# Kernel optimization log

Hardware: AMD Instinct MI355X
Metric: run time of the kernel (lower is better)

Reference implementation:

```python
import jax, jax.numpy as jnp
import numpy as np

D = 640          # feature dim (x_dim)
C = 64           # number of classes
N = 1024         # support samples (16 shots/class)
Q = 2048         # query samples
REG = 0.3        # reg_param


def setup_inputs() -> dict:
    key = jax.random.key(0)
    k0, k1, k2, k3, k4 = jax.random.split(key, 5)
    X = jax.random.normal(k0, (N, D), jnp.float32)
    y = (jnp.arange(N) % C).astype(jnp.int32)          # every class populated
    Xq = jax.random.normal(k1, (Q, D), jnp.float32)
    # learnable prior parameters (perturbed from the torch init so grads are nontrivial)
    m = 0.02 * jax.random.normal(k2, (1, D), jnp.float32)
    kappa = jnp.array([0.1], jnp.float32)
    nu = jnp.array([float(D)], jnp.float32)
    triu_diag = 1.0 + 0.05 * jax.random.normal(k3, (D,), jnp.float32)
    triu_lower = jnp.eye(D, dtype=jnp.float32) + 0.05 * jax.random.normal(k4, (D, D), jnp.float32)
    return {"X": X, "y": y, "Xq": Xq, "m": m, "kappa": kappa, "nu": nu,
            "triu_diag": triu_diag, "triu_lower": triu_lower}


def reference(X, y, Xq, m, kappa, nu, triu_diag, triu_lower):
    # strictly-lower-triangular mask: triu(ones, 1).T
    mask = jnp.triu(jnp.ones((D, D), X.dtype), 1).T
    L = jnp.diag(jnp.abs(triu_diag)) + triu_lower * mask          # Cholesky-like factor
    kappa_ = jnp.abs(kappa[0]) + 1e-6
    nu_ = jnp.maximum(nu[0], D - 1 + 1e-6)

    onehot = jax.nn.one_hot(y, C, dtype=X.dtype)                   # [N, C]
    Nc = onehot.sum(0)                                             # [C]
    mean_c = (onehot.T @ X) / Nc[:, None]                          # [C, D]
    # MAP posterior mean per class
    w = Nc / (kappa_ + Nc)
    mu = (1.0 - w)[:, None] * m + w[:, None] * mean_c              # [C, D]

    # per-class second moment: S_c = sum_{y=c} x x^T (segmented X^T X)
    Xc = onehot.T[:, :, None] * X[None, :, :]                      # [C, N, D]
    S = jnp.einsum('cnd,ne->cde', Xc, X)                           # [C, D, D]

    LLt = L @ L.T
    mm = m.T @ m                                                   # [D, D]
    mu_outer = jnp.einsum('cd,ce->cde', mu, mu)
    sigma = (LLt[None] + S + kappa_ * mm[None]
             - (kappa_ + Nc)[:, None, None] * mu_outer)
    sigma = sigma / (nu_ + Nc + D + 2)[:, None, None]
    sigma_inv = jnp.linalg.inv(sigma)
    sigma_inv = (1.0 - REG) * sigma_inv + REG * jnp.eye(D, dtype=X.dtype)

    # batched Mahalanobis quadratic form: -(x - mu_c)^T Sinv_c (x - mu_c)
    diff = Xq[:, None, :] - mu[None, :, :]                         # [Q, C, D]
    dist = jnp.einsum('qcd,cde,qce->qc', diff, sigma_inv, diff)
    return -dist
```

## Files before the change

kernel.cpp:

```cpp
#include <hip/hip_runtime.h>
#include <hip/hip_bf16.h>


#define D 640
#define C 64
#define NSUP 1024
#define Q 2048
#define KMAX 16
#define R18 18
#define VROWS (C * R18)
#define YROWS 3137
#define YPAD 3200
#define NEXT 704

typedef __attribute__((ext_vector_type(8))) short bf16x8;
typedef __attribute__((ext_vector_type(4))) float floatx4;

__device__ __forceinline__ unsigned short f2bf(float x) {
    unsigned int u = __float_as_uint(x);
    unsigned int r = u + 0x7FFFu + ((u >> 16) & 1u);
    return (unsigned short)(r >> 16);
}

__device__ __forceinline__ void pack4(const float* vv, unsigned short* hp, unsigned short* lp) {
#pragma unroll
    for (int i = 0; i < 4; ++i) {
        unsigned short hb = f2bf(vv[i]);
        float hf = __uint_as_float((unsigned int)hb << 16);
        hp[i] = hb;
        lp[i] = f2bf(vv[i] - hf);
    }
}

__device__ __forceinline__ void rownorm_body(const float* __restrict__ A, int ld,
                                             float* __restrict__ out, int gw, int lane) {
    const float* row = A + (size_t)gw * ld;
    float s = 0.f;
    for (int d = lane; d < D; d += 64) { float v = row[d]; s += v * v; }
#pragma unroll
    for (int off = 32; off; off >>= 1) s += __shfl_xor(s, off);
    if (lane == 0) out[gw] = s;
}

#define BZCH (640 * 640 / 8)
#define AZCH (63 * 640 / 8)
__global__ void k_setup(const int* __restrict__ y, const float* __restrict__ kappa,
                        const float* __restrict__ nu, const float* __restrict__ diag,
                        int* __restrict__ cnt, int* __restrict__ idx,
                        float* __restrict__ sc, float* __restrict__ rd,
                        int* __restrict__ rowmap,
                        unsigned short* __restrict__ Ah, unsigned short* __restrict__ Al,
                        unsigned short* __restrict__ Bh, unsigned short* __restrict__ Bl) {
    int tid = threadIdx.x;
    if (blockIdx.x > 0) {
        int id = (blockIdx.x - 1) * 256 + tid;
        const uint4 z = {0u, 0u, 0u, 0u};
        if (id < BZCH) ((uint4*)Bh)[id] = z;
        else if (id < 2 * BZCH) ((uint4*)Bl)[id - BZCH] = z;
        else if (id < 2 * BZCH + AZCH) ((uint4*)(Ah + (size_t)YROWS * D))[id - 2 * BZCH] = z;
        else if (id < 2 * BZCH + 2 * AZCH) ((uint4*)(Al + (size_t)YROWS * D))[id - 2 * BZCH - AZCH] = z;
        return;
    }
    __shared__ int lc[C];
    if (tid < C) lc[tid] = 0;
    __syncthreads();
    for (int n = tid; n < NSUP; n += 256) {
        int c = y[n];
        int k = atomicAdd(&lc[c], 1);
        if (k < KMAX) idx[c * KMAX + k] = n;
    }
    __syncthreads();
    for (int d = tid; d < D; d += 256) rd[d] = 1.0f / fabsf(diag[d]);
    if (tid < C) {
        int n = lc[tid]; if (n > KMAX) n = KMAX;
        cnt[tid] = n;
        float kap = fabsf(kappa[0]) + 1e-6f;
        float nuv = fmaxf(nu[0], (float)(D - 1) + 1e-6f);
        float Ncf = (float)n;
        sc[64 + tid]  = Ncf / (kap + Ncf);
        sc[128 + tid] = nuv + Ncf + (float)(D + 2);
        sc[192 + tid] = -1.0f / (kap + Ncf);
        if (tid == 0) { sc[0] = kap; sc[1] = nuv; }
    }
    __syncthreads();
    for (int i = tid; i < VROWS; i += 256) {
        int c = i / R18, j = i - c * R18;
        int nc = lc[c] < KMAX ? lc[c] : KMAX;
        int rm;
        if (j == 0) rm = Q + NSUP;
        else if (j <= KMAX) rm = (j - 1 < nc) ? Q + idx[c * KMAX + j - 1] : -1;
        else rm = Q + NSUP + 1 + c;
        rowmap[i] = rm;
    }
}

__global__ __launch_bounds__(256) void k_dinv_mu(
        const float* __restrict__ tlow, const float* __restrict__ rd,
        float* __restrict__ Linv,
        const float* __restrict__ X, const float* __restrict__ m,
        const int* __restrict__ cnt, const int* __restrict__ idx,
        const float* __restrict__ sc, float* __restrict__ mu,
        const float* __restrict__ Xq,
        unsigned short* __restrict__ Ah, unsigned short* __restrict__ Al,
        unsigned short* __restrict__ Bh, unsigned short* __restrict__ Bl,
        float* __restrict__ a0) {
    __shared__ float Lst[128 * 128];
    int tid = threadIdx.x;
    int bid = blockIdx.x;
    if (bid < 160) {
        int b = bid >> 5;
        int j = ((bid & 31) << 2) + (tid >> 6);
        int lane = tid & 63;
        int bB = b * 128;
        {
            float4 tv[16];
            float rv[16];
#pragma unroll
            for (int u = 0; u < 16; ++u) {
                int e = tid + u * 256;
                int c4 = (e & 31) * 4, r = e >> 5;
                tv[u] = *(const float4*)(tlow + (size_t)(bB + r) * D + bB + c4);
                rv[u] = rd[bB + r];
            }
#pragma unroll
            for (int u = 0; u < 16; ++u) {
                int e = tid + u * 256;
                int c4 = (e & 31) * 4, r = e >> 5;
                float vv[4] = {tv[u].x, tv[u].y, tv[u].z, tv[u].w};
#pragma unroll
                for (int t = 0; t < 4; ++t) {
                    int c = c4 + t;
                    float v;
                    if (r == c) v = 1.0f;
                    else if (r > c) v = rv[u] * vv[t];
                    else v = 0.f;
                    Lst[c * 128 + (r ^ (c & 63))] = v;
                }
            }
        }
        __syncthreads();
        float rd0 = rd[bB + lane], rd1 = rd[bB + 64 + lane];
        float acc0 = 0.f, acc1 = 0.f, zz0 = 0.f, zz1 = 0.f;
        for (int i = j; i < 128; ++i) {
            int ri = i >> 6, il = i & 63;
            float av = (ri == 0) ? acc0 : acc1;
            float ai = __shfl(av, il);
            float zi = (i == j) ? __shfl((ri == 0) ? rd0 : rd1, il) : -ai;
            int sw = i & 63;
            float l0 = Lst[i * 128 + (lane ^ sw)];
            float l1 = Lst[i * 128 + 64 + (lane ^ sw)];
            if (lane > i) acc0 += l0 * zi;
            if (64 + lane > i) acc1 += l1 * zi;
            if (lane == i) zz0 = zi;
            if (64 + lane == i) zz1 = zi;
        }
        Linv[(size_t)(bB + lane) * D + bB + j] = zz0;
        Linv[(size_t)(bB + 64 + lane) * D + bB + j] = zz1;
        unsigned short h0 = f2bf(zz0);
        float hf0 = __uint_as_float((unsigned int)h0 << 16);
        Bh[(size_t)(bB + lane) * D + bB + j] = h0;
        Bl[(size_t)(bB + lane) * D + bB + j] = f2bf(zz0 - hf0);
        unsigned short h1 = f2bf(zz1);
        float hf1 = __uint_as_float((unsigned int)h1 << 16);
        Bh[(size_t)(bB + 64 + lane) * D + bB + j] = h1;
        Bl[(size_t)(bB + 64 + lane) * D + bB + j] = f2bf(zz1 - hf1);
    } else if (bid < 320) {
        int u = (bid - 160) * 2 + (tid >> 7);
        int c = u / 5, by = u - c * 5;
        int d = by * 128 + (tid & 127);
        int n = cnt[c];
        float s = 0.f;
        for (int k = 0; k < n; ++k) s += X[(size_t)idx[c * KMAX + k] * D + d];
        float w = sc[64 + c];
        float mean = (n > 0) ? s / (float)n : 0.f;
        float val = (1.f - w) * m[d] + w * mean;
        mu[(size_t)c * D + d] = val;
        unsigned short hb = f2bf(val);
        float hf = __uint_as_float((unsigned int)hb << 16);
        unsigned short lb = f2bf(val - hf);
        Ah[(size_t)(Q + NSUP + 1 + c) * D + d] = hb;
        Al[(size_t)(Q + NSUP + 1 + c) * D + d] = lb;
        Bh[(size_t)(D + c) * D + d] = hb;
        Bl[(size_t)(D + c) * D + d] = lb;
    } else if (bid < 2240) {
        int gid = (bid - 320) * 256 + tid;
        int row = gid / 160, c = (gid - row * 160) * 4;
        float4 v = (row < Q) ? *(const float4*)(Xq + (size_t)row * D + c)
                             : *(const float4*)(X + (size_t)(row - Q) * D + c);
        float vv[4] = {v.x, v.y, v.z, v.w};
        ushort4 h, l;
        pack4(vv, (unsigned short*)&h, (unsigned short*)&l);
        *(ushort4*)(Ah + (size_t)row * D + c) = h;
        *(ushort4*)(Al + (size_t)row * D + c) = l;
    } else if (bid == 2240) {
        if (tid < 160) {
            int c = tid * 4;
            float4 v = *(const float4*)(m + c);
            float vv[4] = {v.x, v.y, v.z, v.w};
            ushort4 h, l;
            pack4(vv, (unsigned short*)&h, (unsigned short*)&l);
            *(ushort4*)(Ah + (size_t)(Q + NSUP) * D + c) = h;
            *(ushort4*)(Al + (size_t)(Q + NSUP) * D + c) = l;
        }
    } else {
        int gw = ((bid - 2241) * 256 + tid) >> 6;
        rownorm_body(Xq, D, a0, gw, tid & 63);
    }
}

__global__ void k_lhat(const float* __restrict__ tlow, const float* __restrict__ Linv,
                       float* __restrict__ Lhat) {
    const int bi_tab[10] = {1, 2, 2, 3, 3, 3, 4, 4, 4, 4};
    const int bk_tab[10] = {0, 0, 1, 0, 1, 2, 0, 1, 2, 3};
    int p = blockIdx.y;
    int bi = bi_tab[p], bk = bk_tab[p];
    int tid = threadIdx.x;
    int c = tid & 127;
    int r = (blockIdx.x << 1) + (tid >> 7);
    const float* drow = Linv + (size_t)(bi * 128 + r) * D + bi * 128;
    const float* lcol = tlow + (size_t)(bi * 128) * D + bk * 128 + c;
    float s = 0.f;
#pragma unroll 4
    for (int t = 0; t < 128; ++t) s += drow[t] * lcol[(size_t)t * D];
    Lhat[(size_t)(bi * 128 + r) * D + bk * 128 + c] = s;
}

template<int B>
__device__ __forceinline__ void linv_chain(const float* __restrict__ Lhat,
                                           float* __restrict__ Linv,
                                           unsigned short* __restrict__ Bh,
                                           unsigned short* __restrict__ Bl,
                                           float S[4][128][20],
                                           int cB, int tid) {
    const int ty = tid >> 2, tx = tid & 3;
    const int r0 = 2 * ty;
    float acc[4 - B][2][4];
#pragma unroll
    for (int a = 0; a < 4 - B; ++a)
#pragma unroll
        for (int rr = 0; rr < 2; ++rr)
#pragma unroll
            for (int cc = 0; cc < 4; ++cc) acc[a][rr][cc] = 0.f;
#pragma unroll
    for (int js = 0; js < 4 - B; ++js) {
        const int j = B + js;
        for (int k0 = 0; k0 < 128; k0 += 8) {
            float svf[8][4];
#pragma unroll
            for (int u = 0; u < 8; ++u) {
                float4 s4 = *(const float4*)&S[js][k0 + u][tx * 4];
                svf[u][0] = s4.x; svf[u][1] = s4.y; svf[u][2] = s4.z; svf[u][3] = s4.w;
            }
#pragma unroll
            for (int a = js; a < 4 - B; ++a) {
                const int i = B + 1 + a;
                const float* p0 = Lhat + (size_t)(i * 128 + r0) * D + j * 128 + k0;
                const float* p1 = p0 + D;
                float4 a00 = *(const float4*)(p0);
                float4 a01 = *(const float4*)(p0 + 4);
                float4 a10 = *(const float4*)(p1);
                float4 a11 = *(const float4*)(p1 + 4);
                float ar0[8] = {a00.x, a00.y, a00.z, a00.w, a01.x, a01.y, a01.z, a01.w};
                float ar1[8] = {a10.x, a10.y, a10.z, a10.w, a11.x, a11.y, a11.z, a11.w};
#pragma unroll
                for (int u = 0; u < 8; ++u) {
#pragma unroll
                    for (int cc = 0; cc < 4; ++cc) {
                        acc[a][0][cc] += ar0[u] * svf[u][cc];
                        acc[a][1][cc] += ar1[u] * svf[u][cc];
                    }
                }
            }
        }
        {
            const int i = j + 1;
#pragma unroll
            for (int rr = 0; rr < 2; ++rr) {
                const int r = r0 + rr;
                float vv[4];
#pragma unroll
                for (int cc = 0; cc < 4; ++cc) vv[cc] = -acc[js][rr][cc];
                float4 v = {vv[0], vv[1], vv[2], vv[3]};
                if (js + 1 < 4 - B) *(float4*)&S[js + 1][r][tx * 4] = v;
                *(float4*)(Linv + (size_t)(i * 128 + r) * D + cB + tx * 4) = v;
                ushort4 hh, ll;
                pack4(vv, (unsigned short*)&hh, (unsigned short*)&ll);
                *(ushort4*)(Bh + (size_t)(i * 128 + r) * D + cB + tx * 4) = hh;
                *(ushort4*)(Bl + (size_t)(i * 128 + r) * D + cB + tx * 4) = ll;
            }
        }
        if (js + 1 < 4 - B) __syncthreads();
    }
}

__global__ __launch_bounds__(256) void k_linv_fill(const float* __restrict__ Lhat,
                                                   float* __restrict__ Linv,
                                                   unsigned short* __restrict__ Bh,
                                                   unsigned short* __restrict__ Bl) {
    __shared__ __align__(16) float S[4][128][20];
    int tid = threadIdx.x;
    int b = blockIdx.x >> 3, strip = blockIdx.x & 7;
    int bB = b * 128, cB = bB + strip * 16;
    {
        int r = tid >> 1, c0 = (tid & 1) * 8;
        const float* src = Linv + (size_t)(bB + r) * D + cB + c0;
        *(float4*)&S[0][r][c0]     = *(const float4*)(src);
        *(float4*)&S[0][r][c0 + 4] = *(const float4*)(src + 4);
    }
    __syncthreads();
    if (b == 0)      linv_chain<0>(Lhat, Linv, Bh, Bl, S, cB, tid);
    else if (b == 1) linv_chain<1>(Lhat, Linv, Bh, Bl, S, cB, tid);
    else if (b == 2) linv_chain<2>(Lhat, Linv, Bh, Bl, S, cB, tid);
    else             linv_chain<3>(Lhat, Linv, Bh, Bl, S, cB, tid);
}

__global__ __launch_bounds__(256) void k_mfma_nt(
        const unsigned short* __restrict__ Ah, const unsigned short* __restrict__ Al,
        const unsigned short* __restrict__ Bh, const unsigned short* __restrict__ Bl,
        float* __restrict__ Out, int M, int N, int ldo,
        unsigned short* __restrict__ Th, unsigned short* __restrict__ Tl) {
    __shared__ unsigned short Ah_s[64 * 32], Al_s[64 * 32];
    __shared__ unsigned short Bh_s[64 * 32], Bl_s[64 * 32];
    int tid = threadIdx.x;
    int rowBase = blockIdx.y * 64, colBase = blockIdx.x * 64;
    int r = tid >> 2, e = (tid & 3) << 3;
    int gr = rowBase + r;
    int gc = colBase + r;
    bool aok = (gr < M), bok = (gc < N);
    int w = tid >> 6, lane = tid & 63, q = lane >> 4, lr = lane & 15;
    int aoff = (16 * w + lr) * 32 + q * 8;
    const uint4 z4 = {0u, 0u, 0u, 0u};
    floatx4 acc[4] = {{0.f, 0.f, 0.f, 0.f}, {0.f, 0.f, 0.f, 0.f},
                      {0.f, 0.f, 0.f, 0.f}, {0.f, 0.f, 0.f, 0.f}};
    for (int kk = 0; kk < D; kk += 32) {
        uint4 vah = aok ? *(const uint4*)(Ah + (size_t)gr * D + kk + e) : z4;
        uint4 val = aok ? *(const uint4*)(Al + (size_t)gr * D + kk + e) : z4;
        uint4 vbh = bok ? *(const uint4*)(Bh + (size_t)gc * D + kk + e) : z4;
        uint4 vbl = bok ? *(const uint4*)(Bl + (size_t)gc * D + kk + e) : z4;
        __syncthreads();
        *(uint4*)(Ah_s + r * 32 + e) = vah;
        *(uint4*)(Al_s + r * 32 + e) = val;
        *(uint4*)(Bh_s + r * 32 + e) = vbh;
        *(uint4*)(Bl_s + r * 32 + e) = vbl;
        __syncthreads();
        bf16x8 ah = *(const bf16x8*)(Ah_s + aoff);
        bf16x8 al = *(const bf16x8*)(Al_s + aoff);
#pragma unroll
        for (int tt = 0; tt < 4; ++tt) {
            int boff = (16 * tt + lr) * 32 + q * 8;
            bf16x8 bh = *(const bf16x8*)(Bh_s + boff);
            bf16x8 bl = *(const bf16x8*)(Bl_s + boff);
            acc[tt] = __builtin_amdgcn_mfma_f32_16x16x32_bf16(ah, bh, acc[tt], 0, 0, 0);
            acc[tt] = __builtin_amdgcn_mfma_f32_16x16x32_bf16(ah, bl, acc[tt], 0, 0, 0);
            acc[tt] = __builtin_amdgcn_mfma_f32_16x16x32_bf16(al, bh, acc[tt], 0, 0, 0);
        }
    }
#pragma unroll
    for (int tt = 0; tt < 4; ++tt) {
        int gc2 = colBase + 16 * tt + lr;
#pragma unroll
        for (int rg = 0; rg < 4; ++rg) {
            int gr2 = rowBase + 16 * w + q * 4 + rg;
            if (gr2 < M && gc2 < N) {
                float v = acc[tt][rg];
                Out[(size_t)gr2 * ldo + gc2] = v;
                if (Th && gc2 < D) {
                    unsigned short hb = f2bf(v);
                    float hf = __uint_as_float((unsigned int)hb << 16);
                    Th[(size_t)gr2 * D + gc2] = hb;
                    Tl[(size_t)gr2 * D + gc2] = f2bf(v - hf);
                }
            }
        }
    }
}

__global__ __launch_bounds__(256) void k_gv(
        const unsigned short* __restrict__ Th, const unsigned short* __restrict__ Tl,
        const int* __restrict__ rowmap, float* __restrict__ G,
        const float* __restrict__ Yt, const float* __restrict__ mu,
        const float* __restrict__ sc, float* __restrict__ at,
        float* __restrict__ h, float* __restrict__ btil,
        float* __restrict__ b0, float* __restrict__ kinv) {
    __shared__ __align__(16) char smem[49344];
    int bid = blockIdx.x, tid = threadIdx.x;
    if (bid < 64) {
        float (*sv)[644] = (float(*)[644])smem;
        float (*aug)[40] = (float(*)[40])(smem + 46368);
        int* rmv = (int*)(smem + 46368 + 2880);
        int c = bid;
        if (tid < R18) rmv[tid] = rowmap[c * R18 + tid];
        __syncthreads();
        {
            int rmu[12];
#pragma unroll
            for (int u = 0; u < 12; ++u) {
                int i = tid + u * 256;
                int r = i / 160;
                rmu[u] = (i < R18 * 160) ? rmv[r] : -1;
            }
            float4 buf[12];
            const float4 z = {0.f, 0.f, 0.f, 0.f};
#pragma unroll
            for (int u = 0; u < 12; ++u) {
                int i = tid + u * 256;
                int d4 = (i - (i / 160) * 160) * 4;
                buf[u] = (rmu[u] >= 0) ? *(const float4*)(Yt + (size_t)rmu[u] * NEXT + d4) : z;
            }
#pragma unroll
            for (int u = 0; u < 12; ++u) {
                int i = tid + u * 256;
                if (i < R18 * 160) {
                    int r = i / 160, d4 = (i - r * 160) * 4;
                    *(float4*)&sv[r][d4] = buf[u];
                }
            }
        }
        __syncthreads();
        if (tid < 171) {
            int i = 0, rem = tid;
            while (rem >= R18 - i) { rem -= R18 - i; ++i; }
            int j = i + rem;
            const float* ri = sv[i];
            const float* rj = sv[j];
            float s0 = 0.f, s1 = 0.f, s2 = 0.f, s3 = 0.f;
#pragma unroll 4
            for (int d = 0; d < D; d += 4) {
                float4 a = *(const float4*)(ri + d);
                float4 bb = *(const float4*)(rj + d);
                s0 += a.x * bb.x; s1 += a.y * bb.y;
                s2 += a.z * bb.z; s3 += a.w * bb.w;
            }
            float s = (s0 + s1) + (s2 + s3);
            aug[i][j] = s;
            if (i != j) aug[j][i] = s;
        }
        for (int i2 = tid; i2 < R18 * R18; i2 += 256)
            aug[i2 / R18][R18 + i2 % R18] = (i2 / R18 == i2 % R18) ? 1.f : 0.f;
        __syncthreads();
        int w = tid >> 6, lane = tid & 63;
        if (w == 1) {
            const float* mc = mu + (size_t)c * D;
            float s = 0.f;
            for (int d = lane; d < D; d += 64) { float v = mc[d]; s += v * v; }
#pragma unroll
            for (int off = 32; off; off >>= 1) s += __shfl_xor(s, off);
            if (lane == 0) b0[c] = s;
        }
        if (w == 0) {
            if (lane < R18) h[c * R18 + lane] = aug[lane][R18 - 1];
            if (lane == 0) btil[c] = aug[R18 - 1][R18 - 1];
            volatile float (*va)[40] = (volatile float (*)[40])aug;
            if (lane == 0) va[0][0] += 1.0f / sc[0];
            else if (lane <= KMAX) va[lane][lane] += 1.0f;
            else if (lane == R18 - 1) va[R18 - 1][R18 - 1] += sc[192 + c];
            __threadfence_block();
            for (int p = 0; p < R18; ++p) {
                float v = (lane >= p && lane < R18) ? fabsf(va[lane][p]) : -1.f;
                int bi = lane;
#pragma unroll
                for (int off = 32; off; off >>= 1) {
                    float ov = __shfl_xor(v, off);
                    int oi = __shfl_xor(bi, off);
                    if (ov > v || (ov == v && oi < bi)) { v = ov; bi = oi; }
                }
                float pv = va[bi][p];
                if (lane < 2 * R18) {
                    float rp = va[bi][lane];
                    if (bi != p) va[bi][lane] = va[p][lane];
                    va[p][lane] = rp / pv;
                }
                __threadfence_block();
                float f  = (lane < R18) ? va[lane][p] : 0.f;
                float pr = (lane < 2 * R18) ? va[p][lane] : 0.f;
#pragma unroll
                for (int it = 0; it < 11; ++it) {
                    int e = lane + it * 64;
                    int r2 = e / 36, cc = e - r2 * 36;
                    float fr = __shfl(f, r2 < R18 ? r2 : 0);
                    float pc = __shfl(pr, cc);
                    if (e < R18 * 2 * R18 && r2 != p) va[r2][cc] -= fr * pc;
                }
                __threadfence_block();
            }
            for (int e = lane; e < R18 * R18; e += 64)
                kinv[(size_t)c * R18 * R18 + e] = va[e / R18][R18 + e % R18];
        }
    } else if (bid < 640) {
        unsigned short* Ah_s = (unsigned short*)smem;
        unsigned short* Al_s = (unsigned short*)(smem + 4096);
        unsigned short* Bh_s = (unsigned short*)(smem + 8192);
        unsigned short* Bl_s = (unsigned short*)(smem + 12288);
        int gb = bid - 64;
        int rowBase = (gb / 18) * 64, colBase = (gb % 18) * 64;
        int r = tid >> 2, e = (tid & 3) << 3;
        int gr = rowBase + r;
        int gc = colBase + r;
        int br = rowmap[gc];
        int w = tid >> 6, lane = tid & 63, q = lane >> 4, lr = lane & 15;
        int aoff = (16 * w + lr) * 32 + q * 8;
        const uint4 z4 = {0u, 0u, 0u, 0u};
        floatx4 acc[4] = {{0.f, 0.f, 0.f, 0.f}, {0.f, 0.f, 0.f, 0.f},
                          {0.f, 0.f, 0.f, 0.f}, {0.f, 0.f, 0.f, 0.f}};
        for (int kk = 0; kk < D; kk += 32) {
            uint4 vah = *(const uint4*)(Th + (size_t)gr * D + kk + e);
            uint4 val = *(const uint4*)(Tl + (size_t)gr * D + kk + e);
            uint4 vbh = (br >= 0) ? *(const uint4*)(Th + (size_t)br * D + kk + e) : z4;
            uint4 vbl = (br >= 0) ? *(const uint4*)(Tl + (size_t)br * D + kk + e) : z4;
            __syncthreads();
            *(uint4*)(Ah_s + r * 32 + e) = vah;
            *(uint4*)(Al_s + r * 32 + e) = val;
            *(uint4*)(Bh_s + r * 32 + e) = vbh;
            *(uint4*)(Bl_s + r * 32 + e) = vbl;
            __syncthreads();
            bf16x8 ah = *(const bf16x8*)(Ah_s + aoff);
            bf16x8 al = *(const bf16x8*)(Al_s + aoff);
#pragma unroll
            for (int tt = 0; tt < 4; ++tt) {
                int boff = (16 * tt + lr) * 32 + q * 8;
                bf16x8 bh = *(const bf16x8*)(Bh_s + boff);
                bf16x8 bl = *(const bf16x8*)(Bl_s + boff);
                acc[tt] = __builtin_amdgcn_mfma_f32_16x16x32_bf16(ah, bh, acc[tt], 0, 0, 0);
                acc[tt] = __builtin_amdgcn_mfma_f32_16x16x32_bf16(ah, bl, acc[tt], 0, 0, 0);
                acc[tt] = __builtin_amdgcn_mfma_f32_16x16x32_bf16(al, bh, acc[tt], 0, 0, 0);
            }
        }
#pragma unroll
        for (int tt = 0; tt < 4; ++tt) {
            int gc2 = colBase + 16 * tt + lr;
#pragma unroll
            for (int rg = 0; rg < 4; ++rg) {
                int gr2 = rowBase + 16 * w + q * 4 + rg;
                G[(size_t)gr2 * VROWS + gc2] = acc[tt][rg];
            }
        }
    } else {
        int gw = ((bid - 640) * 256 + tid) >> 6;
        rownorm_body(Yt, NEXT, at, gw, tid & 63);
    }
}

__global__ void k_epi(const float* __restrict__ G, const float* __restrict__ Yt,
                      const float* __restrict__ at, const float* __restrict__ a0,
                      const float* __restrict__ h, const float* __restrict__ btil,
                      const float* __restrict__ b0, const float* __restrict__ kinv,
                      const float* __restrict__ sc, float* __restrict__ out) {
    __shared__ float lk[R18 * R18], lh[R18];
    __shared__ float ldn, lbt, lb0;
    int c = blockIdx.x, tid = threadIdx.x;
    for (int i = tid; i < R18 * R18; i += 256) lk[i] = kinv[(size_t)c * R18 * R18 + i];
    if (tid < R18) lh[tid] = h[c * R18 + tid];
    if (tid == 0) { ldn = sc[128 + c]; lbt = btil[c]; lb0 = b0[c]; }
    __syncthreads();
    int q = blockIdx.y * 256 + tid;
    const float* Gr = G + (size_t)q * VROWS + c * R18;
    float g[R18];
#pragma unroll
    for (int j = 0; j < R18; ++j) g[j] = Gr[j];
    float ipt = g[R18 - 1];
#pragma unroll
    for (int j = 0; j < R18; ++j) g[j] -= lh[j];
    float corr = 0.f;
#pragma unroll
    for (int i = 0; i < R18; ++i) {
        float s = 0.f;
#pragma unroll
        for (int j = 0; j < R18; ++j) s += lk[i * R18 + j] * g[j];
        corr += g[i] * s;
    }
    float ip0 = Yt[(size_t)q * NEXT + D + c];
    float tt = at[q] - 2.f * ipt + lbt;
    float t0 = a0[q] - 2.f * ip0 + lb0;
    out[(size_t)q * C + c] = -(0.7f * ldn * (tt - corr) + 0.3f * t0);
}

extern "C" void kernel_launch(void* const* d_in, const int* in_sizes, int n_in,
                              void* d_out, int out_size, void* d_ws, size_t ws_size,
                              hipStream_t stream) {
    const float* X     = (const float*)d_in[0];
    const int*   y     = (const int*)d_in[1];
    const float* Xq    = (const float*)d_in[2];
    const float* m     = (const float*)d_in[3];
    const float* kappa = (const float*)d_in[4];
    const float* nu    = (const float*)d_in[5];
    const float* tdiag = (const float*)d_in[6];
    const float* tlow  = (const float*)d_in[7];
    float* out = (float*)d_out;

    char* w = (char*)d_ws;
    auto alloc = [&](size_t bytes) {
        char* p = w;
        w += (bytes + 255) & ~(size_t)255;
        return p;
    };
    int*   cnt    = (int*)alloc(C * 4);
    int*   idx    = (int*)alloc(C * KMAX * 4);
    int*   rowmap = (int*)alloc(VROWS * 4);
    float* sc     = (float*)alloc(256 * 4);
    float* rd     = (float*)alloc(D * 4);
    float* mu     = (float*)alloc((size_t)C * D * 4);
    float* at     = (float*)alloc(Q * 4);
    float* a0     = (float*)alloc(Q * 4);
    float* h      = (float*)alloc(C * R18 * 4);
    float* btil   = (float*)alloc(C * 4);
    float* b0     = (float*)alloc(C * 4);
    float* kinv   = (float*)alloc((size_t)C * R18 * R18 * 4);
    float* Ytout  = (float*)alloc((size_t)YPAD * NEXT * 4);
    unsigned short* Th = (unsigned short*)alloc((size_t)YPAD * D * 2);
    unsigned short* Tl = (unsigned short*)alloc((size_t)YPAD * D * 2);
    unsigned short* Bh = (unsigned short*)alloc((size_t)NEXT * D * 2);
    unsigned short* Bl = (unsigned short*)alloc((size_t)NEXT * D * 2);
    char* wmark = w;
    float* Linv = (float*)alloc((size_t)D * D * 4);
    float* Lhat = (float*)alloc((size_t)D * D * 4);
    unsigned short* Ah = (unsigned short*)alloc((size_t)YPAD * D * 2);
    unsigned short* Al = (unsigned short*)alloc((size_t)YPAD * D * 2);
    w = wmark;
    float* G    = (float*)alloc((size_t)Q * VROWS * 4);

    k_setup<<<441, 256, 0, stream>>>(y, kappa, nu, tdiag, cnt, idx, sc, rd, rowmap,
                                     Ah, Al, Bh, Bl);
    k_dinv_mu<<<2753, 256, 0, stream>>>(tlow, rd, Linv, X, m, cnt, idx, sc, mu,
                                        Xq, Ah, Al, Bh, Bl, a0);
    k_lhat<<<dim3(64, 10), 256, 0, stream>>>(tlow, Linv, Lhat);
    k_linv_fill<<<32, 256, 0, stream>>>(Lhat, Linv, Bh, Bl);
    k_mfma_nt<<<dim3(NEXT / 64, YPAD / 64), 256, 0, stream>>>(
        Ah, Al, Bh, Bl, Ytout, YPAD, NEXT, NEXT, Th, Tl);
    k_gv<<<1152, 256, 0, stream>>>(Th, Tl, rowmap, G, Ytout, mu, sc, at,
                                   h, btil, b0, kinv);
    k_epi<<<dim3(C, Q / 256), 256, 0, stream>>>(G, Ytout, at, a0, h, btil, b0, kinv, sc, out);
}
```

Baseline: 219.1 us.

## Double-buffer padded LDS tiles in MFMA GEMMs and shrink k_gv shared memory

```diff
diff --git a/kernel.cpp b/kernel.cpp
--- a/kernel.cpp
+++ b/kernel.cpp
@@ -12,6 +12,7 @@
 #define YROWS 3137
 #define YPAD 3200
 #define NEXT 704
+#define LP 40
 
 typedef __attribute__((ext_vector_type(8))) short bf16x8;
 typedef __attribute__((ext_vector_type(4))) float floatx4;
@@ -319,8 +320,7 @@
         const unsigned short* __restrict__ Bh, const unsigned short* __restrict__ Bl,
         float* __restrict__ Out, int M, int N, int ldo,
         unsigned short* __restrict__ Th, unsigned short* __restrict__ Tl) {
-    __shared__ unsigned short Ah_s[64 * 32], Al_s[64 * 32];
-    __shared__ unsigned short Bh_s[64 * 32], Bl_s[64 * 32];
+    __shared__ __align__(16) unsigned short SB[2][4][64 * LP];
     int tid = threadIdx.x;
     int rowBase = blockIdx.y * 64, colBase = blockIdx.x * 64;
     int r = tid >> 2, e = (tid & 3) << 3;
@@ -328,33 +328,39 @@
     int gc = colBase + r;
     bool aok = (gr < M), bok = (gc < N);
     int w = tid >> 6, lane = tid & 63, q = lane >> 4, lr = lane & 15;
-    int aoff = (16 * w + lr) * 32 + q * 8;
+    int aoff = (16 * w + lr) * LP + q * 8;
+    int wr = r * LP + e;
     const uint4 z4 = {0u, 0u, 0u, 0u};
     floatx4 acc[4] = {{0.f, 0.f, 0.f, 0.f}, {0.f, 0.f, 0.f, 0.f},
                       {0.f, 0.f, 0.f, 0.f}, {0.f, 0.f, 0.f, 0.f}};
-    for (int kk = 0; kk < D; kk += 32) {
-        uint4 vah = aok ? *(const uint4*)(Ah + (size_t)gr * D + kk + e) : z4;
-        uint4 val = aok ? *(const uint4*)(Al + (size_t)gr * D + kk + e) : z4;
-        uint4 vbh = bok ? *(const uint4*)(Bh + (size_t)gc * D + kk + e) : z4;
-        uint4 vbl = bok ? *(const uint4*)(Bl + (size_t)gc * D + kk + e) : z4;
+    uint4 vah, val, vbh, vbl;
+#define LOADK(kk) { \
+        vah = aok ? *(const uint4*)(Ah + (size_t)gr * D + (kk) + e) : z4; \
+        val = aok ? *(const uint4*)(Al + (size_t)gr * D + (kk) + e) : z4; \
+        vbh = bok ? *(const uint4*)(Bh + (size_t)gc * D + (kk) + e) : z4; \
+        vbl = bok ? *(const uint4*)(Bl + (size_t)gc * D + (kk) + e) : z4; }
+    LOADK(0);
+    for (int step = 0; step < D / 32; ++step) {
+        int cur = step & 1;
+        *(uint4*)(&SB[cur][0][wr]) = vah;
+        *(uint4*)(&SB[cur][1][wr]) = val;
+        *(uint4*)(&SB[cur][2][wr]) = vbh;
+        *(uint4*)(&SB[cur][3][wr]) = vbl;
+        if (step + 1 < D / 32) LOADK((step + 1) * 32);
         __syncthreads();
-        *(uint4*)(Ah_s + r * 32 + e) = vah;
-        *(uint4*)(Al_s + r * 32 + e) = val;
-        *(uint4*)(Bh_s + r * 32 + e) = vbh;
-        *(uint4*)(Bl_s + r * 32 + e) = vbl;
-        __syncthreads();
-        bf16x8 ah = *(const bf16x8*)(Ah_s + aoff);
-        bf16x8 al = *(const bf16x8*)(Al_s + aoff);
+        bf16x8 ah = *(const bf16x8*)(&SB[cur][0][aoff]);
+        bf16x8 al = *(const bf16x8*)(&SB[cur][1][aoff]);
 #pragma unroll
         for (int tt = 0; tt < 4; ++tt) {
-            int boff = (16 * tt + lr) * 32 + q * 8;
-            bf16x8 bh = *(const bf16x8*)(Bh_s + boff);
-            bf16x8 bl = *(const bf16x8*)(Bl_s + boff);
+            int boff = (16 * tt + lr) * LP + q * 8;
+            bf16x8 bh = *(const bf16x8*)(&SB[cur][2][boff]);
+            bf16x8 bl = *(const bf16x8*)(&SB[cur][3][boff]);
             acc[tt] = __builtin_amdgcn_mfma_f32_16x16x32_bf16(ah, bh, acc[tt], 0, 0, 0);
             acc[tt] = __builtin_amdgcn_mfma_f32_16x16x32_bf16(ah, bl, acc[tt], 0, 0, 0);
             acc[tt] = __builtin_amdgcn_mfma_f32_16x16x32_bf16(al, bh, acc[tt], 0, 0, 0);
         }
     }
+#undef LOADK
 #pragma unroll
     for (int tt = 0; tt < 4; ++tt) {
         int gc2 = colBase + 16 * tt + lr;
@@ -382,61 +388,38 @@
         const float* __restrict__ sc, float* __restrict__ at,
         float* __restrict__ h, float* __restrict__ btil,
         float* __restrict__ b0, float* __restrict__ kinv) {
-    __shared__ __align__(16) char smem[49344];
+    __shared__ __align__(16) char smem[40960];
     int bid = blockIdx.x, tid = threadIdx.x;
     if (bid < 64) {
-        float (*sv)[644] = (float(*)[644])smem;
-        float (*aug)[40] = (float(*)[40])(smem + 46368);
-        int* rmv = (int*)(smem + 46368 + 2880);
+        float (*aug)[40] = (float(*)[40])smem;
+        int* rmv = (int*)(smem + 2880);
         int c = bid;
         if (tid < R18) rmv[tid] = rowmap[c * R18 + tid];
-        __syncthreads();
-        {
-            int rmu[12];
-#pragma unroll
-            for (int u = 0; u < 12; ++u) {
-                int i = tid + u * 256;
-                int r = i / 160;
-                rmu[u] = (i < R18 * 160) ? rmv[r] : -1;
-            }
-            float4 buf[12];
-            const float4 z = {0.f, 0.f, 0.f, 0.f};
-#pragma unroll
-            for (int u = 0; u < 12; ++u) {
-                int i = tid + u * 256;
-                int d4 = (i - (i / 160) * 160) * 4;
-                buf[u] = (rmu[u] >= 0) ? *(const float4*)(Yt + (size_t)rmu[u] * NEXT + d4) : z;
-            }
-#pragma unroll
-            for (int u = 0; u < 12; ++u) {
-                int i = tid + u * 256;
-                if (i < R18 * 160) {
-                    int r = i / 160, d4 = (i - r * 160) * 4;
-                    *(float4*)&sv[r][d4] = buf[u];
-                }
-            }
-        }
+        for (int i2 = tid; i2 < R18 * R18; i2 += 256)
+            aug[i2 / R18][R18 + i2 % R18] = (i2 / R18 == i2 % R18) ? 1.f : 0.f;
         __syncthreads();
         if (tid < 171) {
             int i = 0, rem = tid;
             while (rem >= R18 - i) { rem -= R18 - i; ++i; }
             int j = i + rem;
-            const float* ri = sv[i];
-            const float* rj = sv[j];
-            float s0 = 0.f, s1 = 0.f, s2 = 0.f, s3 = 0.f;
+            int rmi = rmv[i], rmj = rmv[j];
+            float s = 0.f;
+            if (rmi >= 0 && rmj >= 0) {
+                const float* ri = Yt + (size_t)rmi * NEXT;
+                const float* rj = Yt + (size_t)rmj * NEXT;
+                float s0 = 0.f, s1 = 0.f, s2 = 0.f, s3 = 0.f;
 #pragma unroll 4
-            for (int d = 0; d < D; d += 4) {
-                float4 a = *(const float4*)(ri + d);
-                float4 bb = *(const float4*)(rj + d);
-                s0 += a.x * bb.x; s1 += a.y * bb.y;
-                s2 += a.z * bb.z; s3 += a.w * bb.w;
-            }
-            float s = (s0 + s1) + (s2 + s3);
+                for (int d = 0; d < D; d += 4) {
+                    float4 a = *(const float4*)(ri + d);
+                    float4 bb = *(const float4*)(rj + d);
+                    s0 += a.x * bb.x; s1 += a.y * bb.y;
+                    s2 += a.z * bb.z; s3 += a.w * bb.w;
+                }
+                s = (s0 + s1) + (s2 + s3);
+            }
             aug[i][j] = s;
             if (i != j) aug[j][i] = s;
         }
-        for (int i2 = tid; i2 < R18 * R18; i2 += 256)
-            aug[i2 / R18][R18 + i2 % R18] = (i2 / R18 == i2 % R18) ? 1.f : 0.f;
         __syncthreads();
         int w = tid >> 6, lane = tid & 63;
         if (w == 1) {
@@ -487,10 +470,7 @@
                 kinv[(size_t)c * R18 * R18 + e] = va[e / R18][R18 + e % R18];
         }
     } else if (bid < 640) {
-        unsigned short* Ah_s = (unsigned short*)smem;
-        unsigned short* Al_s = (unsigned short*)(smem + 4096);
-        unsigned short* Bh_s = (unsigned short*)(smem + 8192);
-        unsigned short* Bl_s = (unsigned short*)(smem + 12288);
+        unsigned short (*SB)[4][64 * LP] = (unsigned short (*)[4][64 * LP])smem;
         int gb = bid - 64;
         int rowBase = (gb / 18) * 64, colBase = (gb % 18) * 64;
         int r = tid >> 2, e = (tid & 3) << 3;
@@ -498,33 +478,39 @@
         int gc = colBase + r;
         int br = rowmap[gc];
         int w = tid >> 6, lane = tid & 63, q = lane >> 4, lr = lane & 15;
-        int aoff = (16 * w + lr) * 32 + q * 8;
+        int aoff = (16 * w + lr) * LP + q * 8;
+        int wr = r * LP + e;
         const uint4 z4 = {0u, 0u, 0u, 0u};
         floatx4 acc[4] = {{0.f, 0.f, 0.f, 0.f}, {0.f, 0.f, 0.f, 0.f},
                           {0.f, 0.f, 0.f, 0.f}, {0.f, 0.f, 0.f, 0.f}};
-        for (int kk = 0; kk < D; kk += 32) {
-            uint4 vah = *(const uint4*)(Th + (size_t)gr * D + kk + e);
-            uint4 val = *(const uint4*)(Tl + (size_t)gr * D + kk + e);
-            uint4 vbh = (br >= 0) ? *(const uint4*)(Th + (size_t)br * D + kk + e) : z4;
-            uint4 vbl = (br >= 0) ? *(const uint4*)(Tl + (size_t)br * D + kk + e) : z4;
+        uint4 vah, val, vbh, vbl;
+#define LOADG(kk) { \
+            vah = *(const uint4*)(Th + (size_t)gr * D + (kk) + e); \
+            val = *(const uint4*)(Tl + (size_t)gr * D + (kk) + e); \
+            vbh = (br >= 0) ? *(const uint4*)(Th + (size_t)br * D + (kk) + e) : z4; \
+            vbl = (br >= 0) ? *(const uint4*)(Tl + (size_t)br * D + (kk) + e) : z4; }
+        LOADG(0);
+        for (int step = 0; step < D / 32; ++step) {
+            int cur = step & 1;
+            *(uint4*)(&SB[cur][0][wr]) = vah;
+            *(uint4*)(&SB[cur][1][wr]) = val;
+            *(uint4*)(&SB[cur][2][wr]) = vbh;
+            *(uint4*)(&SB[cur][3][wr]) = vbl;
+            if (step + 1 < D / 32) LOADG((step + 1) * 32);
             __syncthreads();
-            *(uint4*)(Ah_s + r * 32 + e) = vah;
-            *(uint4*)(Al_s + r * 32 + e) = val;
-            *(uint4*)(Bh_s + r * 32 + e) = vbh;
-            *(uint4*)(Bl_s + r * 32 + e) = vbl;
-            __syncthreads();
-            bf16x8 ah = *(const bf16x8*)(Ah_s + aoff);
-            bf16x8 al = *(const bf16x8*)(Al_s + aoff);
+            bf16x8 ah = *(const bf16x8*)(&SB[cur][0][aoff]);
+            bf16x8 al = *(const bf16x8*)(&SB[cur][1][aoff]);
 #pragma unroll
             for (int tt = 0; tt < 4; ++tt) {
-                int boff = (16 * tt + lr) * 32 + q * 8;
-                bf16x8 bh = *(const bf16x8*)(Bh_s + boff);
-                bf16x8 bl = *(const bf16x8*)(Bl_s + boff);
+                int boff = (16 * tt + lr) * LP + q * 8;
+                bf16x8 bh = *(const bf16x8*)(&SB[cur][2][boff]);
+                bf16x8 bl = *(const bf16x8*)(&SB[cur][3][boff]);
                 acc[tt] = __builtin_amdgcn_mfma_f32_16x16x32_bf16(ah, bh, acc[tt], 0, 0, 0);
                 acc[tt] = __builtin_amdgcn_mfma_f32_16x16x32_bf16(ah, bl, acc[tt], 0, 0, 0);
                 acc[tt] = __builtin_amdgcn_mfma_f32_16x16x32_bf16(al, bh, acc[tt], 0, 0, 0);
             }
         }
+#undef LOADG
 #pragma unroll
         for (int tt = 0; tt < 4; ++tt) {
             int gc2 = colBase + 16 * tt + lr;
```

Result: slower. 227.3 us (+3.7%).
